# Kernel optimization log

Measured on AMD Instinct MI355X. Metric: run time of the kernel, lower is better.

The kernel has to match this reference:

```python
import jax, jax.numpy as jnp
import numpy as np

N, C, HW, D = 16, 512, 3136, 512


def setup_inputs() -> dict:
    key = jax.random.key(0)
    ks = jax.random.split(key, 7)
    s_in = 1.0 / np.sqrt(C)
    return {
        "batch_flat": jax.random.normal(ks[0], (N, C, HW), dtype=jnp.float32),
        "Wq": jax.random.uniform(ks[1], (D, C), jnp.float32, -s_in, s_in),
        "bq": jax.random.uniform(ks[2], (D,), jnp.float32, -s_in, s_in),
        "Wk": jax.random.uniform(ks[3], (D, C), jnp.float32, -s_in, s_in),
        "bk": jax.random.uniform(ks[4], (D,), jnp.float32, -s_in, s_in),
        "Wv": jax.random.uniform(ks[5], (D, C), jnp.float32, -s_in, s_in),
        "bv": jax.random.uniform(ks[6], (D,), jnp.float32, -s_in, s_in),
    }


def reference(batch_flat, Wq, bq, Wk, bk, Wv, bv):
    # batch_flat: [N, C, HW] -> x: [N, HW, C]
    x = jnp.transpose(batch_flat, (0, 2, 1))
    Q = jnp.einsum("nsc,dc->nsd", x, Wq) + bq  # [N, HW, D]
    K = jnp.einsum("nsc,dc->nsd", x, Wk) + bk
    V = jnp.einsum("nsc,dc->nsd", x, Wv) + bv
    # scores = Q^T @ K over the HW axis -> [N, D, D]; softmax over last dim
    att = jax.nn.softmax(jnp.einsum("nsd,nse->nde", Q, K), axis=-1)
    # att @ V^T -> [N, D, HW]
    return jnp.einsum("nde,nse->nds", att, V)
```

## Files before the change

### kernel.cpp

```cpp
#include <hip/hip_runtime.h>

#define NB   16
#define CD   512
#define HW0  3136
#define HWP  3200
#define DD   512

typedef _Float16 half8 __attribute__((ext_vector_type(8)));
typedef _Float16 half2v __attribute__((ext_vector_type(2)));
typedef float    floatx4 __attribute__((ext_vector_type(4)));

__device__ __forceinline__ void load_lds16(const _Float16* g, _Float16* l) {
    __builtin_amdgcn_global_load_lds(
        (__attribute__((address_space(1))) void*)g,
        (__attribute__((address_space(3))) void*)l,
        16, 0, 0);
}

__global__ __launch_bounds__(256) void transpose_cast_kernel(
        const float* __restrict__ in, _Float16* __restrict__ out) {
    __shared__ float tile[128][65];
    const int n  = blockIdx.z;
    const int h0 = blockIdx.x * 64;
    const int c0 = blockIdx.y * 128;
    const int t    = threadIdx.x;
    const int lane = t & 63;
    const int w    = t >> 6;
    const int rsub = lane >> 4;
    const int col4 = (lane & 15) * 4;
    const float* src = in + (long long)n * CD * HW0 + (long long)c0 * HW0 + h0;
    const bool valid = h0 < HW0;

    float4 r[8];
    if (valid) {
#pragma unroll
        for (int j = 0; j < 8; j++) {
            const int row = w * 32 + j * 4 + rsub;
            r[j] = *(const float4*)(src + (long long)row * HW0 + col4);
        }
    } else {
#pragma unroll
        for (int j = 0; j < 8; j++) r[j] = make_float4(0.f, 0.f, 0.f, 0.f);
    }
#pragma unroll
    for (int j = 0; j < 8; j++) {
        const int row = w * 32 + j * 4 + rsub;
        tile[row][col4 + 0] = r[j].x;
        tile[row][col4 + 1] = r[j].y;
        tile[row][col4 + 2] = r[j].z;
        tile[row][col4 + 3] = r[j].w;
    }
    __syncthreads();
    _Float16* dst = out + (long long)n * HWP * CD + (long long)h0 * CD + c0;
#pragma unroll
    for (int j = 0; j < 16; j++) {
        const int i = w * 16 + j;
        half2v v = { (_Float16)tile[2 * lane][i], (_Float16)tile[2 * lane + 1][i] };
        *(half2v*)(dst + (long long)i * CD + 2 * lane) = v;
    }
}

__global__ void convert_w_kernel(const float* __restrict__ wq, const float* __restrict__ wk,
                                 const float* __restrict__ wv, const float* __restrict__ bq,
                                 const float* __restrict__ bk,
                                 _Float16* __restrict__ w2, _Float16* __restrict__ wvh,
                                 float* __restrict__ b2) {
    int i = blockIdx.x * 256 + threadIdx.x;
    if (i < CD * DD) {
        w2[i]           = (_Float16)wq[i];
        w2[CD * DD + i] = (_Float16)wk[i];
        wvh[i]          = (_Float16)wv[i];
    }
    if (i < DD) { b2[i] = bq[i]; b2[DD + i] = bk[i]; }
}

template <int BIAS_MODE, bool OUT_HALF, bool ZERO_PAD, int GX, int GY, int ORDER>
__global__ __launch_bounds__(256, 2)
void gemm_tn(const _Float16* __restrict__ A, const _Float16* __restrict__ B,
             void* __restrict__ Cout, const float* __restrict__ bias,
             int K, int nValid, int ldc,
             long long strideA, long long strideB, long long strideC) {
    constexpr int BM = 128, BN = 128, BK = 32;
    __shared__ _Float16 As[BM * BK];
    __shared__ _Float16 Bs[BN * BK];

    const int tid  = threadIdx.x;
    const int wave = tid >> 6;
    const int lane = tid & 63;

    const int G = gridDim.x;
    const int b = blockIdx.x;
    const int w = (b & 7) * (G >> 3) + (b >> 3);
    int bx, by, bz;
    if (ORDER == 0) { bx = w % GX; int r = w / GX; by = r % GY; bz = r / GY; }
    else            { by = w % GY; int r = w / GY; bx = r % GX; bz = r / GX; }

    const int m0 = bx * BM;
    const int n0 = by * BN;

    const _Float16* Ab = A + (long long)bz * strideA;
    const _Float16* Bb = B + (long long)bz * strideB;

    const int srow = lane >> 2;
    const int scol = (lane & 3) * 8;
    const _Float16* ga0 = Ab + (long long)(m0 + wave * 32 + srow) * K + scol;
    const _Float16* ga1 = ga0 + (long long)16 * K;
    const _Float16* gb0 = Bb + (long long)(n0 + wave * 32 + srow) * K + scol;
    const _Float16* gb1 = gb0 + (long long)16 * K;
    _Float16* lA0 = As + (wave * 32) * BK;
    _Float16* lA1 = As + (wave * 32 + 16) * BK;
    _Float16* lB0 = Bs + (wave * 32) * BK;
    _Float16* lB1 = Bs + (wave * 32 + 16) * BK;

    floatx4 acc[4][4];
#pragma unroll
    for (int i = 0; i < 4; i++)
#pragma unroll
        for (int j = 0; j < 4; j++) acc[i][j] = (floatx4)0.0f;

    const int wm = (wave >> 1) * 64, wn = (wave & 1) * 64;
    const int frow = lane & 15;
    const int fk   = (lane >> 4) * 8;

    for (int k0 = 0; k0 < K; k0 += BK) {
        load_lds16(ga0, lA0); load_lds16(ga1, lA1);
        load_lds16(gb0, lB0); load_lds16(gb1, lB1);
        ga0 += BK; ga1 += BK; gb0 += BK; gb1 += BK;
        __syncthreads();

        half8 af[4], bf[4];
#pragma unroll
        for (int t = 0; t < 4; t++)
            af[t] = *(const half8*)(As + (wm + t * 16 + frow) * BK + fk);
#pragma unroll
        for (int t = 0; t < 4; t++)
            bf[t] = *(const half8*)(Bs + (wn + t * 16 + frow) * BK + fk);
#pragma unroll
        for (int mt = 0; mt < 4; mt++)
#pragma unroll
            for (int nt = 0; nt < 4; nt++)
                acc[mt][nt] = __builtin_amdgcn_mfma_f32_16x16x32_f16(
                    af[mt], bf[nt], acc[mt][nt], 0, 0, 0);
        __syncthreads();
    }

    const int erow = (lane >> 4) * 4;
    const int ecol = lane & 15;
#pragma unroll
    for (int mt = 0; mt < 4; mt++) {
#pragma unroll
        for (int r = 0; r < 4; r++) {
            const int row = m0 + wm + mt * 16 + erow + r;
#pragma unroll
            for (int nt = 0; nt < 4; nt++) {
                const int col = n0 + wn + nt * 16 + ecol;
                float v = acc[mt][nt][r];
                if (BIAS_MODE == 1) v += bias[row];
                if (BIAS_MODE == 2) v += bias[col];
                const bool valid = (col < nValid);
                const long long idx = (long long)bz * strideC + (long long)row * ldc + col;
                if (OUT_HALF) {
                    if (ZERO_PAD) {
                        ((_Float16*)Cout)[idx] = (_Float16)(valid ? v : 0.f);
                    } else if (valid) {
                        ((_Float16*)Cout)[idx] = (_Float16)v;
                    }
                } else {
                    if (ZERO_PAD) {
                        ((float*)Cout)[idx] = valid ? v : 0.f;
                    } else if (valid) {
                        ((float*)Cout)[idx] = v;
                    }
                }
            }
        }
    }
}

__global__ void softmax_kernel(const float* __restrict__ S, _Float16* __restrict__ att) {
    const int row  = blockIdx.x * 4 + (threadIdx.x >> 6);
    const int lane = threadIdx.x & 63;
    const float* src = S + (long long)row * DD;
    float v[8];
#pragma unroll
    for (int i = 0; i < 8; i++) v[i] = src[lane + i * 64];
    float m = v[0];
#pragma unroll
    for (int i = 1; i < 8; i++) m = fmaxf(m, v[i]);
#pragma unroll
    for (int off = 32; off; off >>= 1) m = fmaxf(m, __shfl_xor(m, off, 64));
    float s = 0.f;
#pragma unroll
    for (int i = 0; i < 8; i++) { v[i] = __expf(v[i] - m); s += v[i]; }
#pragma unroll
    for (int off = 32; off; off >>= 1) s += __shfl_xor(s, off, 64);
    const float inv = 1.0f / s;
    _Float16* dst = att + (long long)row * DD;
#pragma unroll
    for (int i = 0; i < 8; i++) dst[lane + i * 64] = (_Float16)(v[i] * inv);
}

extern "C" void kernel_launch(void* const* d_in, const int* in_sizes, int n_in,
                              void* d_out, int out_size, void* d_ws, size_t ws_size,
                              hipStream_t stream) {
    const float* batch = (const float*)d_in[0];
    const float* Wq = (const float*)d_in[1];
    const float* bq = (const float*)d_in[2];
    const float* Wk = (const float*)d_in[3];
    const float* bk = (const float*)d_in[4];
    const float* Wv = (const float*)d_in[5];
    const float* bv = (const float*)d_in[6];

    char* ws = (char*)d_ws;
    const long long XT_B  = (long long)NB * HWP * CD * 2;
    const long long QKT_B = (long long)NB * 2 * DD * HWP * 2;
    const long long VS_B  = (long long)NB * HWP * DD * 2;
    const long long W2_B  = (long long)2 * DD * CD * 2;
    const long long WVH_B = (long long)DD * CD * 2;

    _Float16* Xt  = (_Float16*)(ws);
    _Float16* QKt = (_Float16*)(ws + XT_B);
    _Float16* Vs  = (_Float16*)(ws + XT_B + QKT_B);
    _Float16* W2  = (_Float16*)(ws + XT_B + QKT_B + VS_B);
    _Float16* Wvh = (_Float16*)(ws + XT_B + QKT_B + VS_B + W2_B);
    float*    b2  = (float*)   (ws + XT_B + QKT_B + VS_B + W2_B + WVH_B);
    float*    S   = (float*)(ws);
    _Float16* att = (_Float16*)(ws + (long long)NB * DD * DD * 4);

    convert_w_kernel<<<dim3((CD * DD + 255) / 256), dim3(256), 0, stream>>>(
        Wq, Wk, Wv, bq, bk, W2, Wvh, b2);

    transpose_cast_kernel<<<dim3(HWP / 64, CD / 128, NB), dim3(256), 0, stream>>>(
        batch, Xt);

    gemm_tn<1, true, true, 8, 25, 0><<<dim3(8 * 25 * NB), dim3(256), 0, stream>>>(
        W2, Xt, (void*)QKt, b2, CD, HW0, HWP,
        0LL, (long long)HWP * CD, (long long)2 * DD * HWP);

    gemm_tn<2, true, false, 25, 4, 1><<<dim3(25 * 4 * NB), dim3(256), 0, stream>>>(
        Xt, Wvh, (void*)Vs, bv, CD, DD, DD,
        (long long)HWP * CD, 0LL, (long long)HWP * DD);

    gemm_tn<0, false, false, 4, 4, 0><<<dim3(4 * 4 * NB), dim3(256), 0, stream>>>(
        QKt, QKt + (long long)DD * HWP, (void*)S, nullptr, HWP, DD, DD,
        (long long)2 * DD * HWP, (long long)2 * DD * HWP, (long long)DD * DD);

    softmax_kernel<<<dim3(NB * DD / 4), dim3(256), 0, stream>>>(S, att);

    gemm_tn<0, false, false, 4, 25, 0><<<dim3(4 * 25 * NB), dim3(256), 0, stream>>>(
        att, Vs, d_out, nullptr, DD, HW0, HW0,
        (long long)DD * DD, (long long)HWP * DD, (long long)DD * HW0);
}
```

Measured before the change: 437.0 us.

## Use double-buffered 256x256 GEMM tiles and split-K the scores GEMM

```diff
diff --git a/kernel.cpp b/kernel.cpp
--- a/kernel.cpp
+++ b/kernel.cpp
@@ -3,7 +3,7 @@
 #define NB   16
 #define CD   512
 #define HW0  3136
-#define HWP  3200
+#define HWP  3328
 #define DD   512
 
 typedef _Float16 half8 __attribute__((ext_vector_type(8)));
@@ -75,38 +75,193 @@
 }
 
 template <int BIAS_MODE, bool OUT_HALF, bool ZERO_PAD, int GX, int GY, int ORDER>
-__global__ __launch_bounds__(256, 2)
-void gemm_tn(const _Float16* __restrict__ A, const _Float16* __restrict__ B,
+__global__ __launch_bounds__(512, 2)
+void gemm256(const _Float16* __restrict__ A, const _Float16* __restrict__ B,
              void* __restrict__ Cout, const float* __restrict__ bias,
              int K, int nValid, int ldc,
              long long strideA, long long strideB, long long strideC) {
-    constexpr int BM = 128, BN = 128, BK = 32;
-    __shared__ _Float16 As[BM * BK];
-    __shared__ _Float16 Bs[BN * BK];
+    __shared__ _Float16 sA[2][256 * 64];
+    __shared__ _Float16 sB[2][256 * 64];
 
     const int tid  = threadIdx.x;
     const int wave = tid >> 6;
     const int lane = tid & 63;
 
     const int G = gridDim.x;
-    const int b = blockIdx.x;
-    const int w = (b & 7) * (G >> 3) + (b >> 3);
+    const int bb = blockIdx.x;
+    const int w = (bb & 7) * (G >> 3) + (bb >> 3);
     int bx, by, bz;
     if (ORDER == 0) { bx = w % GX; int r = w / GX; by = r % GY; bz = r / GY; }
     else            { by = w % GY; int r = w / GY; bx = r % GX; bz = r / GX; }
 
-    const int m0 = bx * BM;
-    const int n0 = by * BN;
-
-    const _Float16* Ab = A + (long long)bz * strideA;
-    const _Float16* Bb = B + (long long)bz * strideB;
+    const int m0 = bx * 256, n0 = by * 256;
+    const _Float16* Ab = A + (long long)bz * strideA + (long long)m0 * K;
+    const _Float16* Bb = B + (long long)bz * strideB + (long long)n0 * K;
+
+    const int NT = K >> 6;
+    const int NI = NT >> 1;
+
+    const int sr  = tid >> 3;
+    const long long goff  = (long long)sr * K + (((tid & 7) ^ (sr & 7)) << 3);
+    const long long goff2 = goff + ((long long)K << 6);
+
+#define STG_A(buf, h, kt) if ((kt) < NT) {                                    \
+        const _Float16* g = Ab + ((long long)(h) * 128) * K + ((kt) << 6);    \
+        load_lds16(g + goff,  sA[buf] + (h) * 8192 + tid * 8);                \
+        load_lds16(g + goff2, sA[buf] + (h) * 8192 + tid * 8 + 4096); }
+#define STG_B(buf, h, kt) if ((kt) < NT) {                                    \
+        const _Float16* g = Bb + ((long long)(h) * 128) * K + ((kt) << 6);    \
+        load_lds16(g + goff,  sB[buf] + (h) * 8192 + tid * 8);                \
+        load_lds16(g + goff2, sB[buf] + (h) * 8192 + tid * 8 + 4096); }
+
+    const int frow = lane & 15;
+    const int so0  = ((((lane >> 4) ^ lane) & 7) << 3);
+    const int so1  = so0 ^ 32;
+
+    floatx4 acc[2][2][4][2];
+#pragma unroll
+    for (int q0 = 0; q0 < 2; q0++)
+#pragma unroll
+        for (int q1 = 0; q1 < 2; q1++)
+#pragma unroll
+            for (int q2 = 0; q2 < 4; q2++)
+#pragma unroll
+                for (int q3 = 0; q3 < 2; q3++) acc[q0][q1][q2][q3] = (floatx4)0.0f;
+
+#define MM(MH, NH, I, J, A0_, A1_, B0_, B1_)                                              \
+    acc[MH][NH][I][J] = __builtin_amdgcn_mfma_f32_16x16x32_f16(A0_, B0_, acc[MH][NH][I][J], 0, 0, 0); \
+    acc[MH][NH][I][J] = __builtin_amdgcn_mfma_f32_16x16x32_f16(A1_, B1_, acc[MH][NH][I][J], 0, 0, 0);
+
+#define PHASE(BUF, MH, NH, STAGE, TAIL) {                                                 \
+    const _Float16* aB = sA[BUF] + ((wave >> 2) * 64 + (MH) * 128 + frow) * 64;           \
+    const _Float16* bB = sB[BUF] + ((wave & 3) * 32 + (NH) * 128 + frow) * 64;            \
+    half8 a00 = *(const half8*)(aB +    0 + so0);                                         \
+    half8 a01 = *(const half8*)(aB +    0 + so1);                                         \
+    half8 a10 = *(const half8*)(aB + 1024 + so0);                                         \
+    half8 a11 = *(const half8*)(aB + 1024 + so1);                                         \
+    half8 a20 = *(const half8*)(aB + 2048 + so0);                                         \
+    half8 a21 = *(const half8*)(aB + 2048 + so1);                                         \
+    half8 a30 = *(const half8*)(aB + 3072 + so0);                                         \
+    half8 a31 = *(const half8*)(aB + 3072 + so1);                                         \
+    half8 b0l = *(const half8*)(bB +    0 + so0);                                         \
+    half8 b0h = *(const half8*)(bB +    0 + so1);                                         \
+    half8 b1l = *(const half8*)(bB + 1024 + so0);                                         \
+    half8 b1h = *(const half8*)(bB + 1024 + so1);                                         \
+    STAGE;                                                                                \
+    asm volatile("s_barrier" ::: "memory");                                               \
+    __builtin_amdgcn_s_setprio(1);                                                        \
+    MM(MH, NH, 0, 0, a00, a01, b0l, b0h)                                                  \
+    MM(MH, NH, 0, 1, a00, a01, b1l, b1h)                                                  \
+    MM(MH, NH, 1, 0, a10, a11, b0l, b0h)                                                  \
+    MM(MH, NH, 1, 1, a10, a11, b1l, b1h)                                                  \
+    MM(MH, NH, 2, 0, a20, a21, b0l, b0h)                                                  \
+    MM(MH, NH, 2, 1, a20, a21, b1l, b1h)                                                  \
+    MM(MH, NH, 3, 0, a30, a31, b0l, b0h)                                                  \
+    MM(MH, NH, 3, 1, a30, a31, b1l, b1h)                                                  \
+    __builtin_amdgcn_s_setprio(0);                                                        \
+    TAIL;                                                                                 \
+    asm volatile("s_barrier" ::: "memory");                                               \
+}
+
+#define VM_NONE   {}
+#define VM_TAIL34 { if (i + 1 < NI) asm volatile("s_waitcnt vmcnt(4)" ::: "memory");      \
+                    else            asm volatile("s_waitcnt vmcnt(0)" ::: "memory"); }
+#define VM_TAIL78 { if (i + 1 < NI) asm volatile("s_waitcnt vmcnt(4)" ::: "memory"); }
+
+    STG_A(0, 0, 0); STG_B(0, 0, 0); STG_A(0, 1, 0); STG_B(0, 1, 0);
+    STG_A(1, 0, 1); STG_B(1, 0, 1);
+    asm volatile("s_waitcnt vmcnt(4)" ::: "memory");
+    asm volatile("s_barrier" ::: "memory");
+
+    for (int i = 0; i < NI; i++) {
+        const int T = 2 * i;
+        PHASE(0, 0, 0, STG_A(1, 1, T + 1), VM_NONE)
+        PHASE(0, 0, 1, STG_B(1, 1, T + 1), VM_NONE)
+        PHASE(0, 1, 0, STG_A(0, 0, T + 2), VM_NONE)
+        PHASE(0, 1, 1, STG_B(0, 0, T + 2), VM_TAIL34)
+        PHASE(1, 0, 0, STG_A(0, 1, T + 2), VM_NONE)
+        PHASE(1, 0, 1, STG_B(0, 1, T + 2), VM_NONE)
+        PHASE(1, 1, 0, STG_A(1, 0, T + 3), VM_NONE)
+        PHASE(1, 1, 1, STG_B(1, 0, T + 3), VM_TAIL78)
+    }
+#undef PHASE
+#undef MM
+#undef STG_A
+#undef STG_B
+#undef VM_NONE
+#undef VM_TAIL34
+#undef VM_TAIL78
+
+    const int erow = (lane >> 4) * 4;
+    const int ecol = lane & 15;
+#pragma unroll
+    for (int mh = 0; mh < 2; mh++) {
+#pragma unroll
+        for (int it = 0; it < 4; it++) {
+#pragma unroll
+            for (int r = 0; r < 4; r++) {
+                const int row = m0 + mh * 128 + (wave >> 2) * 64 + it * 16 + erow + r;
+#pragma unroll
+                for (int nh = 0; nh < 2; nh++) {
+#pragma unroll
+                    for (int j = 0; j < 2; j++) {
+                        const int col = n0 + nh * 128 + (wave & 3) * 32 + j * 16 + ecol;
+                        float v = acc[mh][nh][it][j][r];
+                        if (BIAS_MODE == 1) v += bias[row];
+                        if (BIAS_MODE == 2) v += bias[col];
+                        const bool valid = (col < nValid);
+                        const long long idx =
+                            (long long)bz * strideC + (long long)row * ldc + col;
+                        if (OUT_HALF) {
+                            if (ZERO_PAD) {
+                                ((_Float16*)Cout)[idx] = (_Float16)(valid ? v : 0.f);
+                            } else if (valid) {
+                                ((_Float16*)Cout)[idx] = (_Float16)v;
+                            }
+                        } else {
+                            if (ZERO_PAD) {
+                                ((float*)Cout)[idx] = valid ? v : 0.f;
+                            } else if (valid) {
+                                ((float*)Cout)[idx] = v;
+                            }
+                        }
+                    }
+                }
+            }
+        }
+    }
+}
+
+__global__ __launch_bounds__(256, 2)
+void gemm_scores(const _Float16* __restrict__ QK, float* __restrict__ S) {
+    constexpr int BK = 32;
+    constexpr int KH = HWP / 2;
+    __shared__ _Float16 As[128 * BK];
+    __shared__ _Float16 Bs[128 * BK];
+
+    const int tid  = threadIdx.x;
+    const int wave = tid >> 6;
+    const int lane = tid & 63;
+
+    const int G = gridDim.x;
+    const int b = blockIdx.x;
+    const int w = (b & 7) * (G >> 3) + (b >> 3);
+    const int bx = w & 3;
+    const int by = (w >> 2) & 3;
+    const int zz = w >> 4;
+    const int part = zz & 1;
+    const int n    = zz >> 1;
+
+    const int m0 = bx * 128, n0 = by * 128;
+    const _Float16* Ab = QK + (long long)n * (2LL * DD * HWP) + (long long)part * KH;
+    const _Float16* Bb = Ab + (long long)DD * HWP;
 
     const int srow = lane >> 2;
     const int scol = (lane & 3) * 8;
-    const _Float16* ga0 = Ab + (long long)(m0 + wave * 32 + srow) * K + scol;
-    const _Float16* ga1 = ga0 + (long long)16 * K;
-    const _Float16* gb0 = Bb + (long long)(n0 + wave * 32 + srow) * K + scol;
-    const _Float16* gb1 = gb0 + (long long)16 * K;
+    const _Float16* ga0 = Ab + (long long)(m0 + wave * 32 + srow) * HWP + scol;
+    const _Float16* ga1 = ga0 + (long long)16 * HWP;
+    const _Float16* gb0 = Bb + (long long)(n0 + wave * 32 + srow) * HWP + scol;
+    const _Float16* gb1 = gb0 + (long long)16 * HWP;
     _Float16* lA0 = As + (wave * 32) * BK;
     _Float16* lA1 = As + (wave * 32 + 16) * BK;
     _Float16* lB0 = Bs + (wave * 32) * BK;
@@ -122,7 +277,7 @@
     const int frow = lane & 15;
     const int fk   = (lane >> 4) * 8;
 
-    for (int k0 = 0; k0 < K; k0 += BK) {
+    for (int k0 = 0; k0 < KH; k0 += BK) {
         load_lds16(ga0, lA0); load_lds16(ga1, lA1);
         load_lds16(gb0, lB0); load_lds16(gb1, lB1);
         ga0 += BK; ga1 += BK; gb0 += BK; gb1 += BK;
@@ -146,44 +301,28 @@
 
     const int erow = (lane >> 4) * 4;
     const int ecol = lane & 15;
-#pragma unroll
-    for (int mt = 0; mt < 4; mt++) {
+    float* Sb = S + (long long)part * (16LL * DD * DD) + (long long)n * DD * DD;
+#pragma unroll
+    for (int mt = 0; mt < 4; mt++)
 #pragma unroll
         for (int r = 0; r < 4; r++) {
             const int row = m0 + wm + mt * 16 + erow + r;
 #pragma unroll
             for (int nt = 0; nt < 4; nt++) {
                 const int col = n0 + wn + nt * 16 + ecol;
-                float v = acc[mt][nt][r];
-                if (BIAS_MODE == 1) v += bias[row];
-                if (BIAS_MODE == 2) v += bias[col];
-                const bool valid = (col < nValid);
-                const long long idx = (long long)bz * strideC + (long long)row * ldc + col;
-                if (OUT_HALF) {
-                    if (ZERO_PAD) {
-                        ((_Float16*)Cout)[idx] = (_Float16)(valid ? v : 0.f);
-                    } else if (valid) {
-                        ((_Float16*)Cout)[idx] = (_Float16)v;
-                    }
-                } else {
-                    if (ZERO_PAD) {
-                        ((float*)Cout)[idx] = valid ? v : 0.f;
-                    } else if (valid) {
-                        ((float*)Cout)[idx] = v;
-                    }
-                }
+                Sb[(long long)row * DD + col] = acc[mt][nt][r];
             }
         }
-    }
 }
 
 __global__ void softmax_kernel(const float* __restrict__ S, _Float16* __restrict__ att) {
     const int row  = blockIdx.x * 4 + (threadIdx.x >> 6);
     const int lane = threadIdx.x & 63;
-    const float* src = S + (long long)row * DD;
+    const float* s0 = S + (long long)row * DD;
+    const float* s1 = s0 + 16LL * DD * DD;
     float v[8];
 #pragma unroll
-    for (int i = 0; i < 8; i++) v[i] = src[lane + i * 64];
+    for (int i = 0; i < 8; i++) v[i] = s0[lane + i * 64] + s1[lane + i * 64];
     float m = v[0];
 #pragma unroll
     for (int i = 1; i < 8; i++) m = fmaxf(m, v[i]);
@@ -225,7 +364,7 @@
     _Float16* Wvh = (_Float16*)(ws + XT_B + QKT_B + VS_B + W2_B);
     float*    b2  = (float*)   (ws + XT_B + QKT_B + VS_B + W2_B + WVH_B);
     float*    S   = (float*)(ws);
-    _Float16* att = (_Float16*)(ws + (long long)NB * DD * DD * 4);
+    _Float16* att = (_Float16*)(ws + 2LL * NB * DD * DD * 4);
 
     convert_w_kernel<<<dim3((CD * DD + 255) / 256), dim3(256), 0, stream>>>(
         Wq, Wk, Wv, bq, bk, W2, Wvh, b2);
@@ -233,21 +372,19 @@
     transpose_cast_kernel<<<dim3(HWP / 64, CD / 128, NB), dim3(256), 0, stream>>>(
         batch, Xt);
 
-    gemm_tn<1, true, true, 8, 25, 0><<<dim3(8 * 25 * NB), dim3(256), 0, stream>>>(
+    gemm256<1, true, true, 4, 13, 0><<<dim3(4 * 13 * NB), dim3(512), 0, stream>>>(
         W2, Xt, (void*)QKt, b2, CD, HW0, HWP,
         0LL, (long long)HWP * CD, (long long)2 * DD * HWP);
 
-    gemm_tn<2, true, false, 25, 4, 1><<<dim3(25 * 4 * NB), dim3(256), 0, stream>>>(
+    gemm256<2, true, false, 13, 2, 1><<<dim3(13 * 2 * NB), dim3(512), 0, stream>>>(
         Xt, Wvh, (void*)Vs, bv, CD, DD, DD,
         (long long)HWP * CD, 0LL, (long long)HWP * DD);
 
-    gemm_tn<0, false, false, 4, 4, 0><<<dim3(4 * 4 * NB), dim3(256), 0, stream>>>(
-        QKt, QKt + (long long)DD * HWP, (void*)S, nullptr, HWP, DD, DD,
-        (long long)2 * DD * HWP, (long long)2 * DD * HWP, (long long)DD * DD);
+    gemm_scores<<<dim3(4 * 4 * NB * 2), dim3(256), 0, stream>>>(QKt, S);
 
     softmax_kernel<<<dim3(NB * DD / 4), dim3(256), 0, stream>>>(S, att);
 
-    gemm_tn<0, false, false, 4, 25, 0><<<dim3(4 * 25 * NB), dim3(256), 0, stream>>>(
+    gemm256<0, false, false, 2, 13, 0><<<dim3(2 * 13 * NB), dim3(512), 0, stream>>>(
         att, Vs, d_out, nullptr, DD, HW0, HW0,
         (long long)DD * DD, (long long)HWP * DD, (long long)DD * HW0);
 }
```

Result: no change. 444.2 us (+1.6%).

## Swizzle LDS tiles and split-K the scores GEMM with reduction fused into softmax

Applied to the files above, without the earlier changes.

```diff
diff --git a/kernel.cpp b/kernel.cpp
--- a/kernel.cpp
+++ b/kernel.cpp
@@ -102,10 +102,10 @@
     const _Float16* Bb = B + (long long)bz * strideB;
 
     const int srow = lane >> 2;
-    const int scol = (lane & 3) * 8;
-    const _Float16* ga0 = Ab + (long long)(m0 + wave * 32 + srow) * K + scol;
+    const int ssw  = ((lane & 3) ^ (srow & 3)) * 8;
+    const _Float16* ga0 = Ab + (long long)(m0 + wave * 32 + srow) * K + ssw;
     const _Float16* ga1 = ga0 + (long long)16 * K;
-    const _Float16* gb0 = Bb + (long long)(n0 + wave * 32 + srow) * K + scol;
+    const _Float16* gb0 = Bb + (long long)(n0 + wave * 32 + srow) * K + ssw;
     const _Float16* gb1 = gb0 + (long long)16 * K;
     _Float16* lA0 = As + (wave * 32) * BK;
     _Float16* lA1 = As + (wave * 32 + 16) * BK;
@@ -120,7 +120,7 @@
 
     const int wm = (wave >> 1) * 64, wn = (wave & 1) * 64;
     const int frow = lane & 15;
-    const int fk   = (lane >> 4) * 8;
+    const int fk   = (((lane >> 4) ^ frow) & 3) * 8;
 
     for (int k0 = 0; k0 < K; k0 += BK) {
         load_lds16(ga0, lA0); load_lds16(ga1, lA1);
@@ -177,13 +177,97 @@
     }
 }
 
+__global__ __launch_bounds__(256, 2)
+void gemm_scores(const _Float16* __restrict__ QK, float* __restrict__ S) {
+    constexpr int BK = 32;
+    constexpr int KH = HWP / 2;
+    __shared__ _Float16 As[128 * BK];
+    __shared__ _Float16 Bs[128 * BK];
+
+    const int tid  = threadIdx.x;
+    const int wave = tid >> 6;
+    const int lane = tid & 63;
+
+    const int G = gridDim.x;
+    const int b = blockIdx.x;
+    const int w = (b & 7) * (G >> 3) + (b >> 3);
+    const int bx = w & 3;
+    const int by = (w >> 2) & 3;
+    const int zz = w >> 4;
+    const int part = zz & 1;
+    const int n    = zz >> 1;
+
+    const int m0 = bx * 128, n0 = by * 128;
+    const _Float16* Ab = QK + (long long)n * (2LL * DD * HWP) + (long long)part * KH;
+    const _Float16* Bb = Ab + (long long)DD * HWP;
+
+    const int srow = lane >> 2;
+    const int ssw  = ((lane & 3) ^ (srow & 3)) * 8;
+    const _Float16* ga0 = Ab + (long long)(m0 + wave * 32 + srow) * HWP + ssw;
+    const _Float16* ga1 = ga0 + (long long)16 * HWP;
+    const _Float16* gb0 = Bb + (long long)(n0 + wave * 32 + srow) * HWP + ssw;
+    const _Float16* gb1 = gb0 + (long long)16 * HWP;
+    _Float16* lA0 = As + (wave * 32) * BK;
+    _Float16* lA1 = As + (wave * 32 + 16) * BK;
+    _Float16* lB0 = Bs + (wave * 32) * BK;
+    _Float16* lB1 = Bs + (wave * 32 + 16) * BK;
+
+    floatx4 acc[4][4];
+#pragma unroll
+    for (int i = 0; i < 4; i++)
+#pragma unroll
+        for (int j = 0; j < 4; j++) acc[i][j] = (floatx4)0.0f;
+
+    const int wm = (wave >> 1) * 64, wn = (wave & 1) * 64;
+    const int frow = lane & 15;
+    const int fk   = (((lane >> 4) ^ frow) & 3) * 8;
+
+    for (int k0 = 0; k0 < KH; k0 += BK) {
+        load_lds16(ga0, lA0); load_lds16(ga1, lA1);
+        load_lds16(gb0, lB0); load_lds16(gb1, lB1);
+        ga0 += BK; ga1 += BK; gb0 += BK; gb1 += BK;
+        __syncthreads();
+
+        half8 af[4], bf[4];
+#pragma unroll
+        for (int t = 0; t < 4; t++)
+            af[t] = *(const half8*)(As + (wm + t * 16 + frow) * BK + fk);
+#pragma unroll
+        for (int t = 0; t < 4; t++)
+            bf[t] = *(const half8*)(Bs + (wn + t * 16 + frow) * BK + fk);
+#pragma unroll
+        for (int mt = 0; mt < 4; mt++)
+#pragma unroll
+            for (int nt = 0; nt < 4; nt++)
+                acc[mt][nt] = __builtin_amdgcn_mfma_f32_16x16x32_f16(
+                    af[mt], bf[nt], acc[mt][nt], 0, 0, 0);
+        __syncthreads();
+    }
+
+    const int erow = (lane >> 4) * 4;
+    const int ecol = lane & 15;
+    float* Sb = S + (long long)part * (16LL * DD * DD) + (long long)n * DD * DD;
+#pragma unroll
+    for (int mt = 0; mt < 4; mt++)
+#pragma unroll
+        for (int r = 0; r < 4; r++) {
+            const int row = m0 + wm + mt * 16 + erow + r;
+#pragma unroll
+            for (int nt = 0; nt < 4; nt++) {
+                const int col = n0 + wn + nt * 16 + ecol;
+                Sb[(long long)row * DD + col] = acc[mt][nt][r];
+            }
+        }
+}
+
 __global__ void softmax_kernel(const float* __restrict__ S, _Float16* __restrict__ att) {
     const int row  = blockIdx.x * 4 + (threadIdx.x >> 6);
     const int lane = threadIdx.x & 63;
-    const float* src = S + (long long)row * DD;
+    const float* s0 = S + (long long)row * DD;
+    const float* s1 = s0 + 16LL * DD * DD;
     float v[8];
 #pragma unroll
-    for (int i = 0; i < 8; i++) v[i] = src[lane + i * 64];
+    for (int i = 0; i < 8; i++) v[i] = s0[lane + i * 64] + s1[lane + i * 64];
     float m = v[0];
 #pragma unroll
     for (int i = 1; i < 8; i++) m = fmaxf(m, v[i]);
@@ -225,7 +309,7 @@
     _Float16* Wvh = (_Float16*)(ws + XT_B + QKT_B + VS_B + W2_B);
     float*    b2  = (float*)   (ws + XT_B + QKT_B + VS_B + W2_B + WVH_B);
     float*    S   = (float*)(ws);
-    _Float16* att = (_Float16*)(ws + (long long)NB * DD * DD * 4);
+    _Float16* att = (_Float16*)(ws + 2LL * NB * DD * DD * 4);
 
     convert_w_kernel<<<dim3((CD * DD + 255) / 256), dim3(256), 0, stream>>>(
         Wq, Wk, Wv, bq, bk, W2, Wvh, b2);
@@ -241,9 +325,7 @@
         Xt, Wvh, (void*)Vs, bv, CD, DD, DD,
         (long long)HWP * CD, 0LL, (long long)HWP * DD);
 
-    gemm_tn<0, false, false, 4, 4, 0><<<dim3(4 * 4 * NB), dim3(256), 0, stream>>>(
-        QKt, QKt + (long long)DD * HWP, (void*)S, nullptr, HWP, DD, DD,
-        (long long)2 * DD * HWP, (long long)2 * DD * HWP, (long long)DD * DD);
+    gemm_scores<<<dim3(4 * 4 * NB * 2), dim3(256), 0, stream>>>(QKt, S);
 
     softmax_kernel<<<dim3(NB * DD / 4), dim3(256), 0, stream>>>(S, att);
 
```

Result: faster. 401.8 us (-8.1%).
